# Kernel tuning notes

Hardware: AMD Instinct MI355X
Metric: run time of the kernel (lower is better)

The kernel has to match this reference:

```python
import jax, jax.numpy as jnp
import numpy as np

N_NODES = 1_000_000
N_EDGES = 16_000_000
NUM_GRAPHS = 64
LATENT = 128
LAMBDA_LAP = 0.1
LAMBDA_DRIFT = 0.01
LAMBDA_ARAP = 0.1
BETA_WARMUP = 10
BETA_FINAL = 1.0


def setup_inputs() -> dict:
    key = jax.random.key(0)
    k1, k2, k3, k4, k5, k6 = jax.random.split(key, 6)
    return {
        "pred_output": jax.random.normal(k1, (N_NODES, 2), dtype=jnp.float32),
        "target": jax.random.normal(k2, (N_NODES, 2), dtype=jnp.float32),
        "edge_index": jax.random.randint(k3, (2, N_EDGES), 0, N_NODES, dtype=jnp.int32),
        "batch_indices": jnp.sort(jax.random.randint(k4, (N_NODES,), 0, NUM_GRAPHS, dtype=jnp.int32)),
        "mu": jax.random.normal(k5, (NUM_GRAPHS, LATENT), dtype=jnp.float32),
        "logvar": jax.random.normal(k6, (NUM_GRAPHS, LATENT), dtype=jnp.float32),
        "epoch": 5,
    }


def reference(pred_output, target, edge_index, batch_indices, mu, logvar, epoch):
    # reconstruction: MSE, mean over all elements
    recon = jnp.mean((pred_output - target) ** 2)

    # edge gather once; laplacian and ARAP reuse the same diff tensor
    i, j = edge_index[0], edge_index[1]
    diff = pred_output[i] - pred_output[j]                 # [E, 2]
    lap = jnp.sum(diff ** 2) / edge_index.shape[1]

    # drift suppression: per-graph mean displacement via segment_sum
    ones = jnp.ones((pred_output.shape[0],), dtype=pred_output.dtype)
    sums = jax.ops.segment_sum(pred_output, batch_indices, num_segments=NUM_GRAPHS)
    counts = jax.ops.segment_sum(ones, batch_indices, num_segments=NUM_GRAPHS)
    means = sums / counts[:, None]                         # [G, 2]
    drift = jnp.sum(means ** 2) / NUM_GRAPHS

    # ARAP: unbiased variance of edge lengths (torch.var default ddof=1)
    edge_len = jnp.sqrt(jnp.sum(diff ** 2, axis=1))        # [E]
    arap = jnp.var(edge_len, ddof=1)

    # KL divergence, mean over graphs
    kl = jnp.mean(-0.5 * jnp.sum(1.0 + logvar - mu ** 2 - jnp.exp(logvar), axis=1))

    # beta warmup (epoch is a static python int)
    beta = (epoch / BETA_WARMUP) * BETA_FINAL if epoch < BETA_WARMUP else BETA_FINAL

    total = recon + LAMBDA_LAP * lap + LAMBDA_DRIFT * drift + LAMBDA_ARAP * arap + beta * kl
    return total
```

## Files before the change

kernel.cpp:

```cpp
#include <hip/hip_runtime.h>
#include <hip/hip_fp16.h>
#include <math.h>

#define N_NODES    1000000
#define N_EDGES    16000000
#define NUM_GRAPHS 64
#define LATENT     128

#define SH_BASE        8
#define SH_STRIDE      200
#define NSHADOW_BIG    8
#define EDGE_SH_BASE   1608
#define EDGE_NSHADOW   16
#define WS_DOUBLES_TOT 1736
#define WS_DOUBLES_LEGACY 208
#define PACKED_OFFSET_BIG    16384
#define PACKED_OFFSET_LEGACY 2048

typedef int vint4 __attribute__((ext_vector_type(4)));

__global__ void init_ws(double* ws, int n) {
    int t = blockIdx.x * blockDim.x + threadIdx.x;
    if (t < n) ws[t] = 0.0;
}

__global__ void node_kl_pass(const float2* __restrict__ pred,
                             const float2* __restrict__ targ,
                             const int*    __restrict__ batch,
                             const float*  __restrict__ mu,
                             const float*  __restrict__ logvar,
                             double* __restrict__ ws,
                             unsigned* __restrict__ packed,
                             int ns) {
    __shared__ float sgx[NUM_GRAPHS];
    __shared__ float sgy[NUM_GRAPHS];
    __shared__ int   scnt[NUM_GRAPHS];
    __shared__ double smem[8];

    for (int g = threadIdx.x; g < NUM_GRAPHS; g += blockDim.x) {
        sgx[g] = 0.f; sgy[g] = 0.f; scnt[g] = 0;
    }
    __syncthreads();

    double* shbase = ws + SH_BASE + (size_t)(blockIdx.x & (ns - 1)) * SH_STRIDE;

    const int lane   = threadIdx.x & 63;
    const int wid    = threadIdx.x >> 6;
    const int nwaves = (gridDim.x * blockDim.x) >> 6;
    const int gwave  = (blockIdx.x * blockDim.x + threadIdx.x) >> 6;
    const int chunk  = (N_NODES + nwaves - 1) / nwaves;
    const int start  = gwave * chunk;
    const int end    = (start + chunk < N_NODES) ? (start + chunk) : N_NODES;

    float recon = 0.f;
    float sx = 0.f, sy = 0.f;
    int   cnt = 0, bcur = -1;

    for (int n0 = start; n0 < end; n0 += 64) {
        const int n = n0 + lane;
        if (n < end) {
            float2 p = pred[n];
            float2 t = targ[n];
            float dx = p.x - t.x, dy = p.y - t.y;
            recon += dx * dx + dy * dy;

            if (packed) {
                __half2 h = __floats2half2_rn(p.x, p.y);
                packed[n] = *reinterpret_cast<unsigned*>(&h);
            }

            int b = batch[n];
            if (b != bcur) {
                if (cnt != 0) {
                    atomicAdd(&sgx[bcur], sx);
                    atomicAdd(&sgy[bcur], sy);
                    atomicAdd(&scnt[bcur], cnt);
                }
                bcur = b; sx = 0.f; sy = 0.f; cnt = 0;
            }
            sx += p.x; sy += p.y; ++cnt;
        }
    }
    if (cnt != 0) {
        atomicAdd(&sgx[bcur], sx);
        atomicAdd(&sgy[bcur], sy);
        atomicAdd(&scnt[bcur], cnt);
    }

    double r = (double)recon;
    #pragma unroll
    for (int off = 32; off > 0; off >>= 1) r += __shfl_down(r, off);
    if (lane == 0) smem[wid] = r;
    __syncthreads();
    if (threadIdx.x == 0) {
        double tot = 0.0;
        const int nw = blockDim.x >> 6;
        for (int w = 0; w < nw; ++w) tot += smem[w];
        atomicAdd(&shbase[0], tot);
    }

    for (int g = threadIdx.x; g < NUM_GRAPHS; g += blockDim.x) {
        if (scnt[g] != 0) {
            atomicAdd(&shbase[2 + g],   (double)sgx[g]);
            atomicAdd(&shbase[66 + g],  (double)sgy[g]);
            atomicAdd(&shbase[130 + g], (double)scnt[g]);
        }
    }

    if (blockIdx.x == 0) {
        double s = 0.0;
        for (int t = threadIdx.x; t < NUM_GRAPHS * LATENT; t += blockDim.x) {
            float m = mu[t], lv = logvar[t];
            s += (double)(1.0f + lv - m * m - expf(lv));
        }
        #pragma unroll
        for (int off = 32; off > 0; off >>= 1) s += __shfl_down(s, off);
        __syncthreads();
        if (lane == 0) smem[wid] = s;
        __syncthreads();
        if (threadIdx.x == 0) {
            double tot = 0.0;
            const int nw = blockDim.x >> 6;
            for (int w = 0; w < nw; ++w) tot += smem[w];
            atomicAdd(&shbase[1], tot);
        }
    }
}

__device__ __forceinline__ void edge_flush(float s1, float s2, double* ws,
                                           int edge_mode,
                                           double* smem1, double* smem2) {
    double r1 = (double)s1, r2 = (double)s2;
    #pragma unroll
    for (int off = 32; off > 0; off >>= 1) {
        r1 += __shfl_down(r1, off);
        r2 += __shfl_down(r2, off);
    }
    const int lane = threadIdx.x & 63;
    const int wid  = threadIdx.x >> 6;
    if (lane == 0) { smem1[wid] = r1; smem2[wid] = r2; }
    __syncthreads();
    if (threadIdx.x == 0) {
        double t1 = 0.0, t2 = 0.0;
        const int nw = blockDim.x >> 6;
        for (int w = 0; w < nw; ++w) { t1 += smem1[w]; t2 += smem2[w]; }
        if (edge_mode) {
            const int sh = blockIdx.x & (EDGE_NSHADOW - 1);
            atomicAdd(&ws[EDGE_SH_BASE + sh * 8 + 0], t1);
            atomicAdd(&ws[EDGE_SH_BASE + sh * 8 + 1], t2);
        } else {
            atomicAdd(&ws[1], t1);
            atomicAdd(&ws[2], t2);
        }
    }
}

__global__ void edge_pass_packed(const unsigned* __restrict__ packed,
                                 const int* __restrict__ ei,
                                 double* __restrict__ ws,
                                 int edge_mode) {
    __shared__ double smem1[8];
    __shared__ double smem2[8];

    float s1 = 0.f, s2 = 0.f;
    const int gid = blockIdx.x * blockDim.x + threadIdx.x;
    const int stride = gridDim.x * blockDim.x;
    const int ngroups = N_EDGES / 4;
    const vint4* eia = (const vint4*)ei;
    const vint4* eib = (const vint4*)(ei + N_EDGES);

    int g = gid;
    if (g < ngroups) {
        vint4 a = __builtin_nontemporal_load(eia + g);
        vint4 b = __builtin_nontemporal_load(eib + g);
        while (true) {
            unsigned pa0 = packed[a.x], pb0 = packed[b.x];
            unsigned pa1 = packed[a.y], pb1 = packed[b.y];
            unsigned pa2 = packed[a.z], pb2 = packed[b.z];
            unsigned pa3 = packed[a.w], pb3 = packed[b.w];

            const int gn = g + stride;
            const bool more = gn < ngroups;
            vint4 an = {0, 0, 0, 0}, bn = {0, 0, 0, 0};
            if (more) {
                an = __builtin_nontemporal_load(eia + gn);
                bn = __builtin_nontemporal_load(eib + gn);
            }

            {
                __half2 ha = *reinterpret_cast<__half2*>(&pa0);
                __half2 hb = *reinterpret_cast<__half2*>(&pb0);
                float2 fa = __half22float2(ha);
                float2 fb = __half22float2(hb);
                float dx = fa.x - fb.x, dy = fa.y - fb.y;
                float l2 = dx * dx + dy * dy;
                s2 += l2; s1 += sqrtf(l2);
            }
            {
                __half2 ha = *reinterpret_cast<__half2*>(&pa1);
                __half2 hb = *reinterpret_cast<__half2*>(&pb1);
                float2 fa = __half22float2(ha);
                float2 fb = __half22float2(hb);
                float dx = fa.x - fb.x, dy = fa.y - fb.y;
                float l2 = dx * dx + dy * dy;
                s2 += l2; s1 += sqrtf(l2);
            }
            {
                __half2 ha = *reinterpret_cast<__half2*>(&pa2);
                __half2 hb = *reinterpret_cast<__half2*>(&pb2);
                float2 fa = __half22float2(ha);
                float2 fb = __half22float2(hb);
                float dx = fa.x - fb.x, dy = fa.y - fb.y;
                float l2 = dx * dx + dy * dy;
                s2 += l2; s1 += sqrtf(l2);
            }
            {
                __half2 ha = *reinterpret_cast<__half2*>(&pa3);
                __half2 hb = *reinterpret_cast<__half2*>(&pb3);
                float2 fa = __half22float2(ha);
                float2 fb = __half22float2(hb);
                float dx = fa.x - fb.x, dy = fa.y - fb.y;
                float l2 = dx * dx + dy * dy;
                s2 += l2; s1 += sqrtf(l2);
            }

            if (!more) break;
            g = gn; a = an; b = bn;
        }
    }
    edge_flush(s1, s2, ws, edge_mode, smem1, smem2);
}

__global__ void edge_pass_f32(const float2* __restrict__ pred,
                              const int* __restrict__ ei,
                              double* __restrict__ ws,
                              int edge_mode) {
    __shared__ double smem1[8];
    __shared__ double smem2[8];

    float s1 = 0.f, s2 = 0.f;
    const int idx = blockIdx.x * blockDim.x + threadIdx.x;
    const int stride = gridDim.x * blockDim.x;
    for (int e = idx; e < N_EDGES; e += stride) {
        int i = ei[e];
        int j = ei[N_EDGES + e];
        float2 pi = pred[i];
        float2 pj = pred[j];
        float dx = pi.x - pj.x, dy = pi.y - pj.y;
        float l2 = dx * dx + dy * dy;
        s2 += l2;
        s1 += sqrtf(l2);
    }
    edge_flush(s1, s2, ws, edge_mode, smem1, smem2);
}

__global__ void finalize(const double* __restrict__ ws,
                         const int* __restrict__ epoch_p,
                         float* __restrict__ out,
                         int ns, int edge_mode) {
    double recon_sum = 0.0, kl_sum = 0.0;
    for (int s = 0; s < ns; ++s) {
        recon_sum += ws[SH_BASE + s * SH_STRIDE + 0];
        kl_sum    += ws[SH_BASE + s * SH_STRIDE + 1];
    }
    double S1, S2;
    if (edge_mode) {
        S1 = 0.0; S2 = 0.0;
        for (int s = 0; s < EDGE_NSHADOW; ++s) {
            S1 += ws[EDGE_SH_BASE + s * 8 + 0];
            S2 += ws[EDGE_SH_BASE + s * 8 + 1];
        }
    } else {
        S1 = ws[1]; S2 = ws[2];
    }
    double recon = recon_sum / (2.0 * (double)N_NODES);
    double lap  = S2 / (double)N_EDGES;
    double arap = (S2 - S1 * S1 / (double)N_EDGES) / ((double)N_EDGES - 1.0);
    double drift = 0.0;
    for (int g = 0; g < NUM_GRAPHS; ++g) {
        double c = 0.0, sx = 0.0, sy = 0.0;
        for (int s = 0; s < ns; ++s) {
            c  += ws[SH_BASE + s * SH_STRIDE + 130 + g];
            sx += ws[SH_BASE + s * SH_STRIDE + 2 + g];
            sy += ws[SH_BASE + s * SH_STRIDE + 66 + g];
        }
        double mx = sx / c, my = sy / c;
        drift += mx * mx + my * my;
    }
    drift /= (double)NUM_GRAPHS;
    double kl = -0.5 * kl_sum / (double)NUM_GRAPHS;
    int epoch = *epoch_p;
    double beta = (epoch < 10) ? ((double)epoch / 10.0) : 1.0;
    out[0] = (float)(recon + 0.1 * lap + 0.01 * drift + 0.1 * arap + beta * kl);
}

extern "C" void kernel_launch(void* const* d_in, const int* in_sizes, int n_in,
                              void* d_out, int out_size, void* d_ws, size_t ws_size,
                              hipStream_t stream) {
    const float2* pred   = (const float2*)d_in[0];
    const float2* targ   = (const float2*)d_in[1];
    const int*    ei     = (const int*)d_in[2];
    const int*    batch  = (const int*)d_in[3];
    const float*  mu     = (const float*)d_in[4];
    const float*  logvar = (const float*)d_in[5];
    const int*    epoch  = (const int*)d_in[6];
    float* out = (float*)d_out;
    double* ws = (double*)d_ws;

    const size_t packed_bytes = 4ull * N_NODES;
    int ns, edge_mode;
    unsigned* packed;
    if (ws_size >= (size_t)PACKED_OFFSET_BIG + packed_bytes) {
        ns = NSHADOW_BIG; edge_mode = 1;
        packed = (unsigned*)((char*)d_ws + PACKED_OFFSET_BIG);
    } else if (ws_size >= (size_t)PACKED_OFFSET_LEGACY + packed_bytes) {
        ns = 1; edge_mode = 0;
        packed = (unsigned*)((char*)d_ws + PACKED_OFFSET_LEGACY);
    } else {
        ns = 1; edge_mode = 0;
        packed = nullptr;
    }
    const int nz = edge_mode ? WS_DOUBLES_TOT : WS_DOUBLES_LEGACY;

    init_ws<<<(nz + 255) / 256, 256, 0, stream>>>(ws, nz);
    node_kl_pass<<<2048, 256, 0, stream>>>(pred, targ, batch, mu, logvar, ws,
                                           packed, ns);
    if (packed)
        edge_pass_packed<<<2048, 256, 0, stream>>>(packed, ei, ws, edge_mode);
    else
        edge_pass_f32<<<2048, 256, 0, stream>>>(pred, ei, ws, edge_mode);
    finalize<<<1, 1, 0, stream>>>(ws, epoch, out, ns, edge_mode);
}
```

Baseline: 394.0 us.

## Fuse all passes into one cooperative kernel with grid syncs

Replaces the four separate launches (workspace init, node/KL pass, edge pass, finalize) with a single cooperative kernel. It uses grid-wide syncs between phases and has thread 0 compute the final scalar. This aims to remove launch gaps and the trailing single-thread finalize launch. In exchange it pays the cost of grid.sync barriers and needs all 2048 blocks of 256 threads to be co-resident, falling back to the multi-kernel path if the cooperative launch fails.

```diff
diff --git a/kernel.cpp b/kernel.cpp
--- a/kernel.cpp
+++ b/kernel.cpp
@@ -1,4 +1,5 @@
 #include <hip/hip_runtime.h>
+#include <hip/hip_cooperative_groups.h>
 #include <hip/hip_fp16.h>
 #include <math.h>
 
@@ -18,6 +19,234 @@
 #define PACKED_OFFSET_LEGACY 2048
 
 typedef int vint4 __attribute__((ext_vector_type(4)));
+namespace cg = cooperative_groups;
+
+__global__ void __launch_bounds__(256, 8)
+fused_all(const float2* __restrict__ pred,
+          const float2* __restrict__ targ,
+          const int* __restrict__ ei,
+          const int* __restrict__ batch,
+          const float* __restrict__ mu,
+          const float* __restrict__ logvar,
+          const int* __restrict__ epoch_p,
+          float* __restrict__ out,
+          double* __restrict__ ws,
+          unsigned* __restrict__ packed) {
+    cg::grid_group grid = cg::this_grid();
+
+    __shared__ float sgx[NUM_GRAPHS];
+    __shared__ float sgy[NUM_GRAPHS];
+    __shared__ int   scnt[NUM_GRAPHS];
+    __shared__ double smem[8];
+    __shared__ double smem2[8];
+
+    const int tid  = threadIdx.x;
+    const int gtid = blockIdx.x * blockDim.x + tid;
+    const int nthr = gridDim.x * blockDim.x;
+    const int lane = tid & 63;
+    const int wid  = tid >> 6;
+
+    for (int t = gtid; t < WS_DOUBLES_TOT; t += nthr) ws[t] = 0.0;
+    for (int g = tid; g < NUM_GRAPHS; g += blockDim.x) {
+        sgx[g] = 0.f; sgy[g] = 0.f; scnt[g] = 0;
+    }
+    __syncthreads();
+    grid.sync();
+
+    double* shbase = ws + SH_BASE +
+                     (size_t)(blockIdx.x & (NSHADOW_BIG - 1)) * SH_STRIDE;
+    {
+        const int nwaves = nthr >> 6;
+        const int gwave  = gtid >> 6;
+        const int chunk  = (N_NODES + nwaves - 1) / nwaves;
+        const int start  = gwave * chunk;
+        const int end    = (start + chunk < N_NODES) ? (start + chunk)
+                                                     : N_NODES;
+        float recon = 0.f, sx = 0.f, sy = 0.f;
+        int cnt = 0, bcur = -1;
+        for (int n0 = start; n0 < end; n0 += 64) {
+            const int n = n0 + lane;
+            if (n < end) {
+                float2 p = pred[n];
+                float2 t = targ[n];
+                float dx = p.x - t.x, dy = p.y - t.y;
+                recon += dx * dx + dy * dy;
+                __half2 h = __floats2half2_rn(p.x, p.y);
+                packed[n] = *reinterpret_cast<unsigned*>(&h);
+                int b = batch[n];
+                if (b != bcur) {
+                    if (cnt != 0) {
+                        atomicAdd(&sgx[bcur], sx);
+                        atomicAdd(&sgy[bcur], sy);
+                        atomicAdd(&scnt[bcur], cnt);
+                    }
+                    bcur = b; sx = 0.f; sy = 0.f; cnt = 0;
+                }
+                sx += p.x; sy += p.y; ++cnt;
+            }
+        }
+        if (cnt != 0) {
+            atomicAdd(&sgx[bcur], sx);
+            atomicAdd(&sgy[bcur], sy);
+            atomicAdd(&scnt[bcur], cnt);
+        }
+
+        double r = (double)recon;
+        #pragma unroll
+        for (int off = 32; off > 0; off >>= 1) r += __shfl_down(r, off);
+        if (lane == 0) smem[wid] = r;
+        __syncthreads();
+        if (tid == 0) {
+            double tot = 0.0;
+            const int nw = blockDim.x >> 6;
+            for (int w = 0; w < nw; ++w) tot += smem[w];
+            atomicAdd(&shbase[0], tot);
+        }
+        for (int g = tid; g < NUM_GRAPHS; g += blockDim.x) {
+            if (scnt[g] != 0) {
+                atomicAdd(&shbase[2 + g],   (double)sgx[g]);
+                atomicAdd(&shbase[66 + g],  (double)sgy[g]);
+                atomicAdd(&shbase[130 + g], (double)scnt[g]);
+            }
+        }
+        if (blockIdx.x == 0) {
+            double s = 0.0;
+            for (int t = tid; t < NUM_GRAPHS * LATENT; t += blockDim.x) {
+                float m = mu[t], lv = logvar[t];
+                s += (double)(1.0f + lv - m * m - expf(lv));
+            }
+            #pragma unroll
+            for (int off = 32; off > 0; off >>= 1) s += __shfl_down(s, off);
+            __syncthreads();
+            if (lane == 0) smem[wid] = s;
+            __syncthreads();
+            if (tid == 0) {
+                double tot = 0.0;
+                const int nw = blockDim.x >> 6;
+                for (int w = 0; w < nw; ++w) tot += smem[w];
+                atomicAdd(&shbase[1], tot);
+            }
+        }
+    }
+    grid.sync();
+
+    {
+        float s1 = 0.f, s2 = 0.f;
+        const int stride = nthr;
+        const int ngroups = N_EDGES / 4;
+        const vint4* eia = (const vint4*)ei;
+        const vint4* eib = (const vint4*)(ei + N_EDGES);
+
+        int g = gtid;
+        if (g < ngroups) {
+            vint4 a = __builtin_nontemporal_load(eia + g);
+            vint4 b = __builtin_nontemporal_load(eib + g);
+            while (true) {
+                unsigned pa0 = packed[a.x], pb0 = packed[b.x];
+                unsigned pa1 = packed[a.y], pb1 = packed[b.y];
+                unsigned pa2 = packed[a.z], pb2 = packed[b.z];
+                unsigned pa3 = packed[a.w], pb3 = packed[b.w];
+
+                const int gn = g + stride;
+                const bool more = gn < ngroups;
+                vint4 an = {0, 0, 0, 0}, bn = {0, 0, 0, 0};
+                if (more) {
+                    an = __builtin_nontemporal_load(eia + gn);
+                    bn = __builtin_nontemporal_load(eib + gn);
+                }
+                {
+                    __half2 ha = *reinterpret_cast<__half2*>(&pa0);
+                    __half2 hb = *reinterpret_cast<__half2*>(&pb0);
+                    float2 fa = __half22float2(ha);
+                    float2 fb = __half22float2(hb);
+                    float dx = fa.x - fb.x, dy = fa.y - fb.y;
+                    float l2 = dx * dx + dy * dy;
+                    s2 += l2; s1 += sqrtf(l2);
+                }
+                {
+                    __half2 ha = *reinterpret_cast<__half2*>(&pa1);
+                    __half2 hb = *reinterpret_cast<__half2*>(&pb1);
+                    float2 fa = __half22float2(ha);
+                    float2 fb = __half22float2(hb);
+                    float dx = fa.x - fb.x, dy = fa.y - fb.y;
+                    float l2 = dx * dx + dy * dy;
+                    s2 += l2; s1 += sqrtf(l2);
+                }
+                {
+                    __half2 ha = *reinterpret_cast<__half2*>(&pa2);
+                    __half2 hb = *reinterpret_cast<__half2*>(&pb2);
+                    float2 fa = __half22float2(ha);
+                    float2 fb = __half22float2(hb);
+                    float dx = fa.x - fb.x, dy = fa.y - fb.y;
+                    float l2 = dx * dx + dy * dy;
+                    s2 += l2; s1 += sqrtf(l2);
+                }
+                {
+                    __half2 ha = *reinterpret_cast<__half2*>(&pa3);
+                    __half2 hb = *reinterpret_cast<__half2*>(&pb3);
+                    float2 fa = __half22float2(ha);
+                    float2 fb = __half22float2(hb);
+                    float dx = fa.x - fb.x, dy = fa.y - fb.y;
+                    float l2 = dx * dx + dy * dy;
+                    s2 += l2; s1 += sqrtf(l2);
+                }
+                if (!more) break;
+                g = gn; a = an; b = bn;
+            }
+        }
+        double r1 = (double)s1, r2 = (double)s2;
+        #pragma unroll
+        for (int off = 32; off > 0; off >>= 1) {
+            r1 += __shfl_down(r1, off);
+            r2 += __shfl_down(r2, off);
+        }
+        if (lane == 0) { smem[wid] = r1; smem2[wid] = r2; }
+        __syncthreads();
+        if (tid == 0) {
+            double t1 = 0.0, t2 = 0.0;
+            const int nw = blockDim.x >> 6;
+            for (int w = 0; w < nw; ++w) { t1 += smem[w]; t2 += smem2[w]; }
+            const int sh = blockIdx.x & (EDGE_NSHADOW - 1);
+            atomicAdd(&ws[EDGE_SH_BASE + sh * 8 + 0], t1);
+            atomicAdd(&ws[EDGE_SH_BASE + sh * 8 + 1], t2);
+        }
+    }
+    grid.sync();
+
+    if (gtid == 0) {
+        double recon_sum = 0.0, kl_sum = 0.0;
+        for (int s = 0; s < NSHADOW_BIG; ++s) {
+            recon_sum += ws[SH_BASE + s * SH_STRIDE + 0];
+            kl_sum    += ws[SH_BASE + s * SH_STRIDE + 1];
+        }
+        double S1 = 0.0, S2 = 0.0;
+        for (int s = 0; s < EDGE_NSHADOW; ++s) {
+            S1 += ws[EDGE_SH_BASE + s * 8 + 0];
+            S2 += ws[EDGE_SH_BASE + s * 8 + 1];
+        }
+        double recon = recon_sum / (2.0 * (double)N_NODES);
+        double lap  = S2 / (double)N_EDGES;
+        double arap = (S2 - S1 * S1 / (double)N_EDGES)
+                      / ((double)N_EDGES - 1.0);
+        double drift = 0.0;
+        for (int g = 0; g < NUM_GRAPHS; ++g) {
+            double c = 0.0, sx = 0.0, sy = 0.0;
+            for (int s = 0; s < NSHADOW_BIG; ++s) {
+                c  += ws[SH_BASE + s * SH_STRIDE + 130 + g];
+                sx += ws[SH_BASE + s * SH_STRIDE + 2 + g];
+                sy += ws[SH_BASE + s * SH_STRIDE + 66 + g];
+            }
+            double mx = sx / c, my = sy / c;
+            drift += mx * mx + my * my;
+        }
+        drift /= (double)NUM_GRAPHS;
+        double kl = -0.5 * kl_sum / (double)NUM_GRAPHS;
+        int epoch = *epoch_p;
+        double beta = (epoch < 10) ? ((double)epoch / 10.0) : 1.0;
+        out[0] = (float)(recon + 0.1 * lap + 0.01 * drift + 0.1 * arap
+                         + beta * kl);
+    }
+}
 
 __global__ void init_ws(double* ws, int n) {
     int t = blockIdx.x * blockDim.x + threadIdx.x;
@@ -52,10 +281,8 @@
     const int start  = gwave * chunk;
     const int end    = (start + chunk < N_NODES) ? (start + chunk) : N_NODES;
 
-    float recon = 0.f;
-    float sx = 0.f, sy = 0.f;
-    int   cnt = 0, bcur = -1;
-
+    float recon = 0.f, sx = 0.f, sy = 0.f;
+    int cnt = 0, bcur = -1;
     for (int n0 = start; n0 < end; n0 += 64) {
         const int n = n0 + lane;
         if (n < end) {
@@ -63,12 +290,10 @@
             float2 t = targ[n];
             float dx = p.x - t.x, dy = p.y - t.y;
             recon += dx * dx + dy * dy;
-
             if (packed) {
                 __half2 h = __floats2half2_rn(p.x, p.y);
                 packed[n] = *reinterpret_cast<unsigned*>(&h);
             }
-
             int b = batch[n];
             if (b != bcur) {
                 if (cnt != 0) {
@@ -98,7 +323,6 @@
         for (int w = 0; w < nw; ++w) tot += smem[w];
         atomicAdd(&shbase[0], tot);
     }
-
     for (int g = threadIdx.x; g < NUM_GRAPHS; g += blockDim.x) {
         if (scnt[g] != 0) {
             atomicAdd(&shbase[2 + g],   (double)sgx[g]);
@@ -106,7 +330,6 @@
             atomicAdd(&shbase[130 + g], (double)scnt[g]);
         }
     }
-
     if (blockIdx.x == 0) {
         double s = 0.0;
         for (int t = threadIdx.x; t < NUM_GRAPHS * LATENT; t += blockDim.x) {
@@ -186,7 +409,6 @@
                 an = __builtin_nontemporal_load(eia + gn);
                 bn = __builtin_nontemporal_load(eib + gn);
             }
-
             {
                 __half2 ha = *reinterpret_cast<__half2*>(&pa0);
                 __half2 hb = *reinterpret_cast<__half2*>(&pb0);
@@ -223,7 +445,6 @@
                 float l2 = dx * dx + dy * dy;
                 s2 += l2; s1 += sqrtf(l2);
             }
-
             if (!more) break;
             g = gn; a = an; b = bn;
         }
@@ -308,21 +529,29 @@
     double* ws = (double*)d_ws;
 
     const size_t packed_bytes = 4ull * N_NODES;
-    int ns, edge_mode;
-    unsigned* packed;
+
     if (ws_size >= (size_t)PACKED_OFFSET_BIG + packed_bytes) {
-        ns = NSHADOW_BIG; edge_mode = 1;
-        packed = (unsigned*)((char*)d_ws + PACKED_OFFSET_BIG);
-    } else if (ws_size >= (size_t)PACKED_OFFSET_LEGACY + packed_bytes) {
-        ns = 1; edge_mode = 0;
-        packed = (unsigned*)((char*)d_ws + PACKED_OFFSET_LEGACY);
-    } else {
-        ns = 1; edge_mode = 0;
-        packed = nullptr;
-    }
-    const int nz = edge_mode ? WS_DOUBLES_TOT : WS_DOUBLES_LEGACY;
-
-    init_ws<<<(nz + 255) / 256, 256, 0, stream>>>(ws, nz);
+        unsigned* packed = (unsigned*)((char*)d_ws + PACKED_OFFSET_BIG);
+        void* args[] = { (void*)&pred, (void*)&targ, (void*)&ei,
+                         (void*)&batch, (void*)&mu, (void*)&logvar,
+                         (void*)&epoch, (void*)&out, (void*)&ws,
+                         (void*)&packed };
+        hipError_t err = hipLaunchCooperativeKernel(
+            (const void*)fused_all, dim3(2048), dim3(256), args, 0, stream);
+        if (err == hipSuccess) return;
+        init_ws<<<(WS_DOUBLES_TOT + 255) / 256, 256, 0, stream>>>(
+            ws, WS_DOUBLES_TOT);
+        node_kl_pass<<<2048, 256, 0, stream>>>(pred, targ, batch, mu, logvar,
+                                               ws, packed, NSHADOW_BIG);
+        edge_pass_packed<<<2048, 256, 0, stream>>>(packed, ei, ws, 1);
+        finalize<<<1, 1, 0, stream>>>(ws, epoch, out, NSHADOW_BIG, 1);
+        return;
+    }
+
+    int ns = 1, edge_mode = 0;
+    unsigned* packed = (ws_size >= (size_t)PACKED_OFFSET_LEGACY + packed_bytes)
+        ? (unsigned*)((char*)d_ws + PACKED_OFFSET_LEGACY) : (unsigned*)nullptr;
+    init_ws<<<1, 256, 0, stream>>>(ws, WS_DOUBLES_LEGACY);
     node_kl_pass<<<2048, 256, 0, stream>>>(pred, targ, batch, mu, logvar, ws,
                                            packed, ns);
     if (packed)
```

After: 1.170 ms. 2.97x slower.
